# Kernel optimization log

Hardware: AMD Instinct MI355X
Metric: run time of the kernel (lower is better)

The kernel has to match this reference:

```python
import jax, jax.numpy as jnp
import numpy as np

B, T, IN, H, P = 1024, 100, 1, 256, 0.5


def _lstm_scan(xs, h0, c0, Wih, Whh, bih, bhh, mask_h, mask_in=None):
    """Run an LSTMCell over time with variational dropout masks.
    xs: [T, B, D]. mask_h multiplies the recurrent hidden state (as in the
    original: cell(x_t, (h * mask1, c))); mask_in (optional) multiplies input.
    PyTorch LSTMCell gate order: i, f, g, o."""
    b = bih + bhh

    def step(carry, xt):
        h, c = carry
        xin = xt if mask_in is None else xt * mask_in
        g = xin @ Wih.T + (h * mask_h) @ Whh.T + b  # [B, 4H]
        i, f, gg, o = jnp.split(g, 4, axis=-1)
        c = jax.nn.sigmoid(f) * c + jax.nn.sigmoid(i) * jnp.tanh(gg)
        h = jax.nn.sigmoid(o) * jnp.tanh(c)
        return (h, c), h

    _, hs = jax.lax.scan(step, (h0, c0), xs)
    return hs  # [T, B, H]


def setup_inputs() -> dict:
    key = jax.random.key(0)
    ks = jax.random.split(key, 24)
    s = 1.0 / np.sqrt(H)

    def u(k, shape):
        return jax.random.uniform(k, shape, jnp.float32, -s, s)

    inp = {"x0": jax.random.normal(ks[0], (B, T, IN), jnp.float32)}
    names = ["1f", "1b", "2f", "2b"]
    in_sizes = [2 * IN, 2 * IN, 2 * H, 2 * H]
    i = 1
    for n, d in zip(names, in_sizes):
        inp[f"Wih{n}"] = u(ks[i], (4 * H, d)); i += 1
        inp[f"Whh{n}"] = u(ks[i], (4 * H, H)); i += 1
        inp[f"bih{n}"] = u(ks[i], (4 * H,)); i += 1
        inp[f"bhh{n}"] = u(ks[i], (4 * H,)); i += 1
    inp["Wout"] = u(ks[17], (IN, 2 * H))
    inp["bout"] = u(ks[18], (IN,))
    # Variational dropout masks (Bernoulli(1 - dropout_prob)), per set_dropout(batch)
    def bern(k, shape):
        return (jax.random.uniform(k, shape) > P).astype(jnp.float32)
    inp["mask1"] = bern(ks[19], (B, H))
    inp["mask2"] = bern(ks[20], (B, 2 * H))
    inp["mask3"] = bern(ks[21], (B, H))
    inp["mask4"] = bern(ks[22], (B, 1, 2 * H))
    return inp


def reference(x0,
              Wih1f, Whh1f, bih1f, bhh1f,
              Wih1b, Whh1b, bih1b, bhh1b,
              Wih2f, Whh2f, bih2f, bhh2f,
              Wih2b, Whh2b, bih2b, bhh2b,
              Wout, bout, mask1, mask2, mask3, mask4):
    batch = x0.shape[0]
    m = x0.mean(axis=1, keepdims=True)                       # [B, 1, IN]
    x = jnp.concatenate([x0 - m, jnp.broadcast_to(m, x0.shape)], axis=2)  # [B, T, 2*IN]
    xs = jnp.swapaxes(x, 0, 1)                               # [T, B, 2*IN]

    h0 = jnp.zeros((batch, H), x0.dtype)
    c0 = jnp.zeros((batch, H), x0.dtype)

    # Layer 1, forward and backward in time (backward outputs NOT re-flipped,
    # faithful to the original which stacks them in reversed-visit order).
    hf = _lstm_scan(xs, h0, c0, Wih1f, Whh1f, bih1f, bhh1f, mask1)
    hb = _lstm_scan(xs[::-1], h0, c0, Wih1b, Whh1b, bih1b, bhh1b, mask1)
    p1 = jnp.concatenate([hf, hb], axis=-1)                  # [T, B, 2H]

    # Layer 2 with input mask2 and recurrent mask3
    h2f = _lstm_scan(p1, h0, c0, Wih2f, Whh2f, bih2f, bhh2f, mask3, mask_in=mask2)
    h2b = _lstm_scan(p1[::-1], h0, c0, Wih2b, Whh2b, bih2b, bhh2b, mask3, mask_in=mask2)
    p2 = jnp.concatenate([h2f, h2b], axis=-1)                # [T, B, 2H]

    pa = jnp.swapaxes(p2, 0, 1)                              # [B, T, 2H]
    pred = (pa * mask4) @ Wout.T + bout                      # [B, T, IN]
    return pred + m
```

## Files before the change

### kernel.cpp

```cpp
#include <hip/hip_runtime.h>
#include <cstdint>
#include <cstddef>

#define B_  1024
#define T_  100
#define H_  256

typedef _Float16 f16x8 __attribute__((ext_vector_type(8)));
typedef float    f32x16 __attribute__((ext_vector_type(16)));

__device__ __forceinline__ float sigm(float x){ return 1.0f/(1.0f + __expf(-x)); }
__device__ __forceinline__ float tanh_(float x){ return 1.0f - 2.0f/(1.0f + __expf(2.0f*x)); }

#define W_WHH1F 0
#define W_WHH1B 262144
#define W_WIH2F 524288
#define W_WIH2B 1048576
#define W_WHH2F 1572864
#define W_WHH2B 1835008
#define W_TOTAL 2097152

__device__ __forceinline__ void gemm_chunk(
    f32x16 acc[4],
    const _Float16* __restrict__ Asrc, int a_stride,
    const _Float16* __restrict__ Wsrc, int w_stride,
    _Float16* Alds,
    int b0, int j0, int lane, int rw, int cw)
{
  const int t = threadIdx.x;
  #pragma unroll
  for (int i = 0; i < 8; i++){
    int u   = t + 256*i;
    int row = u >> 5;
    int c8  = u & 31;
    uint4 v = *(const uint4*)(Asrc + (size_t)(b0 + row)*a_stride + c8*8);
    *(uint4*)(Alds + row*264 + c8*8) = v;
  }
  __syncthreads();
  const _Float16* arow = Alds + (rw*32 + (lane & 31))*264 + (lane >> 5)*8;
  const int nbase = j0 + cw*32 + (lane & 31);
  const int kq    = (lane >> 5)*8;
  #pragma unroll
  for (int kk = 0; kk < 16; kk++){
    f16x8 a = *(const f16x8*)(arow + kk*16);
    #pragma unroll
    for (int g = 0; g < 4; g++){
      const _Float16* wp = Wsrc + (size_t)(g*256 + nbase)*w_stride + kk*16 + kq;
      f16x8 bw = *(const f16x8*)wp;
      acc[g] = __builtin_amdgcn_mfma_f32_32x32x16_f16(a, bw, acc[g], 0, 0, 0);
    }
  }
  __syncthreads();
}

__global__ void conv_weights(const float* __restrict__ Whh1f, const float* __restrict__ Whh1b,
                             const float* __restrict__ Wih2f, const float* __restrict__ Wih2b,
                             const float* __restrict__ Whh2f, const float* __restrict__ Whh2b,
                             _Float16* __restrict__ dst)
{
  int idx = blockIdx.x*256 + threadIdx.x;
  if      (idx < W_WHH1B) dst[idx] = (_Float16)Whh1f[idx];
  else if (idx < W_WIH2F) dst[idx] = (_Float16)Whh1b[idx - W_WHH1B];
  else if (idx < W_WIH2B) dst[idx] = (_Float16)Wih2f[idx - W_WIH2F];
  else if (idx < W_WHH2F) dst[idx] = (_Float16)Wih2b[idx - W_WIH2B];
  else if (idx < W_WHH2B) dst[idx] = (_Float16)Whh2f[idx - W_WHH2F];
  else if (idx < W_TOTAL) dst[idx] = (_Float16)Whh2b[idx - W_WHH2B];
}

__global__ __launch_bounds__(256, 2)
void l1_step(const _Float16* __restrict__ wpool,
             const float* __restrict__ Wih_f,
             const float* __restrict__ Wih_b,
             const float* __restrict__ bih_f,
             const float* __restrict__ bhh_f,
             const float* __restrict__ bih_b,
             const float* __restrict__ bhh_b,
             const float* __restrict__ x0,
             const float* __restrict__ mvec,
             const float* __restrict__ mask1,
             const float* __restrict__ mask2,
             const _Float16* __restrict__ hm_in,
             _Float16* __restrict__ hm_out,
             float* __restrict__ cbuf,
             _Float16* __restrict__ p1m,
             int s)
{
  __shared__ __align__(16) _Float16 Alds[64*264];
  const int dir = blockIdx.z;
  const int b0  = blockIdx.x*64, j0 = blockIdx.y*64;
  const int lane = threadIdx.x & 63;
  const int w = threadIdx.x >> 6, rw = w >> 1, cw = w & 1;

  f32x16 acc[4];
  #pragma unroll
  for (int g = 0; g < 4; g++)
    #pragma unroll
    for (int e = 0; e < 16; e++) acc[g][e] = 0.0f;

  const _Float16* Whh = wpool + (dir ? W_WHH1B : W_WHH1F);
  gemm_chunk(acc, hm_in + (size_t)dir*B_*H_, H_, Whh, H_, Alds, b0, j0, lane, rw, cw);

  const int tin = dir ? (T_-1-s) : s;
  const float* Wih = dir ? Wih_b : Wih_f;
  const float* bih = dir ? bih_b : bih_f;
  const float* bhh = dir ? bhh_b : bhh_f;
  const int jj = j0 + cw*32 + (lane & 31);

  float wi0[4], wi1[4], bs[4];
  #pragma unroll
  for (int g = 0; g < 4; g++){
    int n = g*256 + jj;
    wi0[g] = Wih[n*2 + 0];
    wi1[g] = Wih[n*2 + 1];
    bs[g]  = bih[n] + bhh[n];
  }
  float* cp = cbuf + (size_t)dir*B_*H_;
  _Float16* hmo = hm_out + (size_t)dir*B_*H_;

  #pragma unroll
  for (int r = 0; r < 16; r++){
    int row = (r & 3) + 8*(r >> 2) + 4*(lane >> 5);
    int b   = b0 + rw*32 + row;
    float mv = mvec[b];
    float xd = x0[b*T_ + tin] - mv;
    float gi = acc[0][r] + xd*wi0[0] + mv*wi1[0] + bs[0];
    float gf = acc[1][r] + xd*wi0[1] + mv*wi1[1] + bs[1];
    float gg = acc[2][r] + xd*wi0[2] + mv*wi1[2] + bs[2];
    float go = acc[3][r] + xd*wi0[3] + mv*wi1[3] + bs[3];
    float ii = sigm(gi), ff = sigm(gf), g2 = tanh_(gg), oo = sigm(go);
    size_t cidx = (size_t)b*H_ + jj;
    float cn = ff*cp[cidx] + ii*g2;
    cp[cidx] = cn;
    float h = oo*tanh_(cn);
    hmo[cidx] = (_Float16)(h * mask1[cidx]);
    p1m[((size_t)s*B_ + b)*512 + dir*256 + jj] =
        (_Float16)(h * mask2[(size_t)b*512 + dir*256 + jj]);
  }
}

__global__ __launch_bounds__(256, 2)
void l2_step(const _Float16* __restrict__ wpool,
             const float* __restrict__ bih_f,
             const float* __restrict__ bhh_f,
             const float* __restrict__ bih_b,
             const float* __restrict__ bhh_b,
             const _Float16* __restrict__ p1m,
             const float* __restrict__ mask3,
             const float* __restrict__ mask4,
             const float* __restrict__ Wout,
             const _Float16* __restrict__ hm_in,
             _Float16* __restrict__ hm_out,
             float* __restrict__ cbuf,
             float* __restrict__ pred,
             int s)
{
  __shared__ __align__(16) _Float16 Alds[64*264];
  const int dir = blockIdx.z;
  const int b0  = blockIdx.x*64, j0 = blockIdx.y*64;
  const int lane = threadIdx.x & 63;
  const int w = threadIdx.x >> 6, rw = w >> 1, cw = w & 1;

  f32x16 acc[4];
  #pragma unroll
  for (int g = 0; g < 4; g++)
    #pragma unroll
    for (int e = 0; e < 16; e++) acc[g][e] = 0.0f;

  const int tin = dir ? (T_-1-s) : s;
  const _Float16* Wih = wpool + (dir ? W_WIH2B : W_WIH2F);
  const _Float16* Whh = wpool + (dir ? W_WHH2B : W_WHH2F);
  const _Float16* Ain = p1m + (size_t)tin*B_*512;

  gemm_chunk(acc, Ain,       512, Wih,       512, Alds, b0, j0, lane, rw, cw);
  gemm_chunk(acc, Ain + 256, 512, Wih + 256, 512, Alds, b0, j0, lane, rw, cw);
  gemm_chunk(acc, hm_in + (size_t)dir*B_*H_, H_, Whh, H_, Alds, b0, j0, lane, rw, cw);

  const float* bih = dir ? bih_b : bih_f;
  const float* bhh = dir ? bhh_b : bhh_f;
  const int jj = j0 + cw*32 + (lane & 31);
  float bs[4];
  #pragma unroll
  for (int g = 0; g < 4; g++)
    bs[g] = bih[g*256 + jj] + bhh[g*256 + jj];
  float wo = Wout[dir*256 + jj];
  float* cp = cbuf + (size_t)dir*B_*H_;
  _Float16* hmo = hm_out + (size_t)dir*B_*H_;

  #pragma unroll
  for (int r = 0; r < 16; r++){
    int row = (r & 3) + 8*(r >> 2) + 4*(lane >> 5);
    int b   = b0 + rw*32 + row;
    float gi = acc[0][r] + bs[0];
    float gf = acc[1][r] + bs[1];
    float gg = acc[2][r] + bs[2];
    float go = acc[3][r] + bs[3];
    float ii = sigm(gi), ff = sigm(gf), g2 = tanh_(gg), oo = sigm(go);
    size_t cidx = (size_t)b*H_ + jj;
    float cn = ff*cp[cidx] + ii*g2;
    cp[cidx] = cn;
    float h = oo*tanh_(cn);
    hmo[cidx] = (_Float16)(h * mask3[cidx]);
    float contrib = h * mask4[(size_t)b*512 + dir*256 + jj] * wo;
    contrib += __shfl_xor(contrib, 16);
    contrib += __shfl_xor(contrib, 8);
    contrib += __shfl_xor(contrib, 4);
    contrib += __shfl_xor(contrib, 2);
    contrib += __shfl_xor(contrib, 1);
    if ((lane & 31) == 0) atomicAdd(&pred[(size_t)b*T_ + s], contrib);
  }
}

__global__ void prep_kernel(const float* __restrict__ x0,
                            float* __restrict__ mvec)
{
  int b = blockIdx.x*blockDim.x + threadIdx.x;
  if (b < B_){
    float ssum = 0.0f;
    for (int t = 0; t < T_; t++) ssum += x0[b*T_ + t];
    mvec[b] = ssum * (1.0f / T_);
  }
}

__global__ void final_kernel(const float* __restrict__ pred,
                             const float* __restrict__ mvec,
                             const float* __restrict__ bout,
                             float* __restrict__ out)
{
  int idx = blockIdx.x*256 + threadIdx.x;
  if (idx < B_*T_){
    int b = idx / T_;
    out[idx] = pred[idx] + bout[0] + mvec[b];
  }
}

extern "C" void kernel_launch(void* const* d_in, const int* in_sizes, int n_in,
                              void* d_out, int out_size, void* d_ws, size_t ws_size,
                              hipStream_t stream)
{
  (void)in_sizes; (void)n_in; (void)out_size; (void)ws_size;
  const float* x0    = (const float*)d_in[0];
  const float* Wih1f = (const float*)d_in[1];
  const float* Whh1f = (const float*)d_in[2];
  const float* bih1f = (const float*)d_in[3];
  const float* bhh1f = (const float*)d_in[4];
  const float* Wih1b = (const float*)d_in[5];
  const float* Whh1b = (const float*)d_in[6];
  const float* bih1b = (const float*)d_in[7];
  const float* bhh1b = (const float*)d_in[8];
  const float* Wih2f = (const float*)d_in[9];
  const float* Whh2f = (const float*)d_in[10];
  const float* bih2f = (const float*)d_in[11];
  const float* bhh2f = (const float*)d_in[12];
  const float* Wih2b = (const float*)d_in[13];
  const float* Whh2b = (const float*)d_in[14];
  const float* bih2b = (const float*)d_in[15];
  const float* bhh2b = (const float*)d_in[16];
  const float* Wout  = (const float*)d_in[17];
  const float* bout  = (const float*)d_in[18];
  const float* mask1 = (const float*)d_in[19];
  const float* mask2 = (const float*)d_in[20];
  const float* mask3 = (const float*)d_in[21];
  const float* mask4 = (const float*)d_in[22];
  float* out = (float*)d_out;

  char* ws = (char*)d_ws;
  size_t off = 0;
  _Float16* wpool = (_Float16*)(ws + off); off += (size_t)W_TOTAL*2;
  _Float16* p1m  = (_Float16*)(ws + off); off += (size_t)T_*B_*512*2;
  float* pred = (float*)(ws + off); off += (size_t)B_*T_*4;
  float* mvec = (float*)(ws + off); off += (size_t)B_*4;
  float* cbuf = (float*)(ws + off); off += (size_t)2*2*B_*H_*4;
  _Float16* hm = (_Float16*)(ws + off); off += (size_t)2*2*2*B_*H_*2;

  hipMemsetAsync(pred, 0, (size_t)B_*T_*4, stream);
  hipMemsetAsync(cbuf, 0, (size_t)2*2*B_*H_*4 + (size_t)2*2*2*B_*H_*2, stream);

  conv_weights<<<dim3(W_TOTAL/256), dim3(256), 0, stream>>>(
      Whh1f, Whh1b, Wih2f, Wih2b, Whh2f, Whh2b, wpool);
  prep_kernel<<<dim3(4), dim3(256), 0, stream>>>(x0, mvec);

  dim3 grid(16, 4, 2), blk(256);
  float* cL1 = cbuf;
  float* cL2 = cbuf + (size_t)2*B_*H_;
  _Float16* hmL1 = hm;
  _Float16* hmL2 = hm + (size_t)2*2*B_*H_;
  const size_t pp = (size_t)2*B_*H_;

  for (int s = 0; s < T_; s++){
    l1_step<<<grid, blk, 0, stream>>>(wpool, Wih1f, Wih1b,
        bih1f, bhh1f, bih1b, bhh1b, x0, mvec, mask1, mask2,
        hmL1 + (size_t)(s & 1)*pp, hmL1 + (size_t)((s + 1) & 1)*pp, cL1, p1m, s);
  }
  for (int s = 0; s < T_; s++){
    l2_step<<<grid, blk, 0, stream>>>(wpool,
        bih2f, bhh2f, bih2b, bhh2b, p1m, mask3, mask4, Wout,
        hmL2 + (size_t)(s & 1)*pp, hmL2 + (size_t)((s + 1) & 1)*pp, cL2, pred, s);
  }
  final_kernel<<<dim3((B_*T_ + 255)/256), dim3(256), 0, stream>>>(pred, mvec, bout, out);
}
```

Before: 5.193 ms.

## Replace per-timestep kernel launches with a persistent kernel using group barriers

The 200 per-step launches for the two LSTM layers are replaced by a single persistent kernel of 256 blocks of 128 threads. Each block owns a 32-row batch tile and a 64-column hidden tile. Blocks sharing a batch tile and direction synchronise each step through atomic counters in global memory, so launch overhead and device-wide step boundaries go away. A global barrier separates layer 1 from layer 2. The smaller tiles halve per-block reuse of the weights, and correctness depends on all 256 blocks being co-resident.

```diff
diff --git a/kernel.cpp b/kernel.cpp
--- a/kernel.cpp
+++ b/kernel.cpp
@@ -19,39 +19,6 @@
 #define W_WHH2F 1572864
 #define W_WHH2B 1835008
 #define W_TOTAL 2097152
-
-__device__ __forceinline__ void gemm_chunk(
-    f32x16 acc[4],
-    const _Float16* __restrict__ Asrc, int a_stride,
-    const _Float16* __restrict__ Wsrc, int w_stride,
-    _Float16* Alds,
-    int b0, int j0, int lane, int rw, int cw)
-{
-  const int t = threadIdx.x;
-  #pragma unroll
-  for (int i = 0; i < 8; i++){
-    int u   = t + 256*i;
-    int row = u >> 5;
-    int c8  = u & 31;
-    uint4 v = *(const uint4*)(Asrc + (size_t)(b0 + row)*a_stride + c8*8);
-    *(uint4*)(Alds + row*264 + c8*8) = v;
-  }
-  __syncthreads();
-  const _Float16* arow = Alds + (rw*32 + (lane & 31))*264 + (lane >> 5)*8;
-  const int nbase = j0 + cw*32 + (lane & 31);
-  const int kq    = (lane >> 5)*8;
-  #pragma unroll
-  for (int kk = 0; kk < 16; kk++){
-    f16x8 a = *(const f16x8*)(arow + kk*16);
-    #pragma unroll
-    for (int g = 0; g < 4; g++){
-      const _Float16* wp = Wsrc + (size_t)(g*256 + nbase)*w_stride + kk*16 + kq;
-      f16x8 bw = *(const f16x8*)wp;
-      acc[g] = __builtin_amdgcn_mfma_f32_32x32x16_f16(a, bw, acc[g], 0, 0, 0);
-    }
-  }
-  __syncthreads();
-}
 
 __global__ void conv_weights(const float* __restrict__ Whh1f, const float* __restrict__ Whh1b,
                              const float* __restrict__ Wih2f, const float* __restrict__ Wih2b,
@@ -67,152 +34,7 @@
   else if (idx < W_TOTAL) dst[idx] = (_Float16)Whh2b[idx - W_WHH2B];
 }
 
-__global__ __launch_bounds__(256, 2)
-void l1_step(const _Float16* __restrict__ wpool,
-             const float* __restrict__ Wih_f,
-             const float* __restrict__ Wih_b,
-             const float* __restrict__ bih_f,
-             const float* __restrict__ bhh_f,
-             const float* __restrict__ bih_b,
-             const float* __restrict__ bhh_b,
-             const float* __restrict__ x0,
-             const float* __restrict__ mvec,
-             const float* __restrict__ mask1,
-             const float* __restrict__ mask2,
-             const _Float16* __restrict__ hm_in,
-             _Float16* __restrict__ hm_out,
-             float* __restrict__ cbuf,
-             _Float16* __restrict__ p1m,
-             int s)
-{
-  __shared__ __align__(16) _Float16 Alds[64*264];
-  const int dir = blockIdx.z;
-  const int b0  = blockIdx.x*64, j0 = blockIdx.y*64;
-  const int lane = threadIdx.x & 63;
-  const int w = threadIdx.x >> 6, rw = w >> 1, cw = w & 1;
-
-  f32x16 acc[4];
-  #pragma unroll
-  for (int g = 0; g < 4; g++)
-    #pragma unroll
-    for (int e = 0; e < 16; e++) acc[g][e] = 0.0f;
-
-  const _Float16* Whh = wpool + (dir ? W_WHH1B : W_WHH1F);
-  gemm_chunk(acc, hm_in + (size_t)dir*B_*H_, H_, Whh, H_, Alds, b0, j0, lane, rw, cw);
-
-  const int tin = dir ? (T_-1-s) : s;
-  const float* Wih = dir ? Wih_b : Wih_f;
-  const float* bih = dir ? bih_b : bih_f;
-  const float* bhh = dir ? bhh_b : bhh_f;
-  const int jj = j0 + cw*32 + (lane & 31);
-
-  float wi0[4], wi1[4], bs[4];
-  #pragma unroll
-  for (int g = 0; g < 4; g++){
-    int n = g*256 + jj;
-    wi0[g] = Wih[n*2 + 0];
-    wi1[g] = Wih[n*2 + 1];
-    bs[g]  = bih[n] + bhh[n];
-  }
-  float* cp = cbuf + (size_t)dir*B_*H_;
-  _Float16* hmo = hm_out + (size_t)dir*B_*H_;
-
-  #pragma unroll
-  for (int r = 0; r < 16; r++){
-    int row = (r & 3) + 8*(r >> 2) + 4*(lane >> 5);
-    int b   = b0 + rw*32 + row;
-    float mv = mvec[b];
-    float xd = x0[b*T_ + tin] - mv;
-    float gi = acc[0][r] + xd*wi0[0] + mv*wi1[0] + bs[0];
-    float gf = acc[1][r] + xd*wi0[1] + mv*wi1[1] + bs[1];
-    float gg = acc[2][r] + xd*wi0[2] + mv*wi1[2] + bs[2];
-    float go = acc[3][r] + xd*wi0[3] + mv*wi1[3] + bs[3];
-    float ii = sigm(gi), ff = sigm(gf), g2 = tanh_(gg), oo = sigm(go);
-    size_t cidx = (size_t)b*H_ + jj;
-    float cn = ff*cp[cidx] + ii*g2;
-    cp[cidx] = cn;
-    float h = oo*tanh_(cn);
-    hmo[cidx] = (_Float16)(h * mask1[cidx]);
-    p1m[((size_t)s*B_ + b)*512 + dir*256 + jj] =
-        (_Float16)(h * mask2[(size_t)b*512 + dir*256 + jj]);
-  }
-}
-
-__global__ __launch_bounds__(256, 2)
-void l2_step(const _Float16* __restrict__ wpool,
-             const float* __restrict__ bih_f,
-             const float* __restrict__ bhh_f,
-             const float* __restrict__ bih_b,
-             const float* __restrict__ bhh_b,
-             const _Float16* __restrict__ p1m,
-             const float* __restrict__ mask3,
-             const float* __restrict__ mask4,
-             const float* __restrict__ Wout,
-             const _Float16* __restrict__ hm_in,
-             _Float16* __restrict__ hm_out,
-             float* __restrict__ cbuf,
-             float* __restrict__ pred,
-             int s)
-{
-  __shared__ __align__(16) _Float16 Alds[64*264];
-  const int dir = blockIdx.z;
-  const int b0  = blockIdx.x*64, j0 = blockIdx.y*64;
-  const int lane = threadIdx.x & 63;
-  const int w = threadIdx.x >> 6, rw = w >> 1, cw = w & 1;
-
-  f32x16 acc[4];
-  #pragma unroll
-  for (int g = 0; g < 4; g++)
-    #pragma unroll
-    for (int e = 0; e < 16; e++) acc[g][e] = 0.0f;
-
-  const int tin = dir ? (T_-1-s) : s;
-  const _Float16* Wih = wpool + (dir ? W_WIH2B : W_WIH2F);
-  const _Float16* Whh = wpool + (dir ? W_WHH2B : W_WHH2F);
-  const _Float16* Ain = p1m + (size_t)tin*B_*512;
-
-  gemm_chunk(acc, Ain,       512, Wih,       512, Alds, b0, j0, lane, rw, cw);
-  gemm_chunk(acc, Ain + 256, 512, Wih + 256, 512, Alds, b0, j0, lane, rw, cw);
-  gemm_chunk(acc, hm_in + (size_t)dir*B_*H_, H_, Whh, H_, Alds, b0, j0, lane, rw, cw);
-
-  const float* bih = dir ? bih_b : bih_f;
-  const float* bhh = dir ? bhh_b : bhh_f;
-  const int jj = j0 + cw*32 + (lane & 31);
-  float bs[4];
-  #pragma unroll
-  for (int g = 0; g < 4; g++)
-    bs[g] = bih[g*256 + jj] + bhh[g*256 + jj];
-  float wo = Wout[dir*256 + jj];
-  float* cp = cbuf + (size_t)dir*B_*H_;
-  _Float16* hmo = hm_out + (size_t)dir*B_*H_;
-
-  #pragma unroll
-  for (int r = 0; r < 16; r++){
-    int row = (r & 3) + 8*(r >> 2) + 4*(lane >> 5);
-    int b   = b0 + rw*32 + row;
-    float gi = acc[0][r] + bs[0];
-    float gf = acc[1][r] + bs[1];
-    float gg = acc[2][r] + bs[2];
-    float go = acc[3][r] + bs[3];
-    float ii = sigm(gi), ff = sigm(gf), g2 = tanh_(gg), oo = sigm(go);
-    size_t cidx = (size_t)b*H_ + jj;
-    float cn = ff*cp[cidx] + ii*g2;
-    cp[cidx] = cn;
-    float h = oo*tanh_(cn);
-    hmo[cidx] = (_Float16)(h * mask3[cidx]);
-    float contrib = h * mask4[(size_t)b*512 + dir*256 + jj] * wo;
-    contrib += __shfl_xor(contrib, 16);
-    contrib += __shfl_xor(contrib, 8);
-    contrib += __shfl_xor(contrib, 4);
-    contrib += __shfl_xor(contrib, 2);
-    contrib += __shfl_xor(contrib, 1);
-    if ((lane & 31) == 0) atomicAdd(&pred[(size_t)b*T_ + s], contrib);
-  }
-}
-
-__global__ void prep_kernel(const float* __restrict__ x0,
-                            float* __restrict__ mvec)
-{
+__global__ void prep_kernel(const float* __restrict__ x0, float* __restrict__ mvec){
   int b = blockIdx.x*blockDim.x + threadIdx.x;
   if (b < B_){
     float ssum = 0.0f;
@@ -221,15 +43,187 @@
   }
 }
 
-__global__ void final_kernel(const float* __restrict__ pred,
-                             const float* __restrict__ mvec,
-                             const float* __restrict__ bout,
-                             float* __restrict__ out)
-{
+__global__ void final_kernel(const float* __restrict__ pred, const float* __restrict__ mvec,
+                             const float* __restrict__ bout, float* __restrict__ out){
   int idx = blockIdx.x*256 + threadIdx.x;
   if (idx < B_*T_){
     int b = idx / T_;
     out[idx] = pred[idx] + bout[0] + mvec[b];
+  }
+}
+
+struct PP {
+  const float *x0, *Wih1f, *Wih1b, *b1f_ih, *b1f_hh, *b1b_ih, *b1b_hh;
+  const float *b2f_ih, *b2f_hh, *b2b_ih, *b2b_hh;
+  const float *Wout, *mask1, *mask2, *mask3, *mask4;
+  const _Float16 *wpool;
+  _Float16 *p1m, *hm1, *hm2;
+  float *cbuf1, *cbuf2, *pred, *mvec;
+  unsigned *ctr1, *ctr2, *ctrF;
+};
+
+__device__ __forceinline__ void bar_wait(unsigned* c, unsigned target){
+  __syncthreads();
+  if (threadIdx.x == 0){
+    __threadfence();
+    __hip_atomic_fetch_add(c, 1u, __ATOMIC_RELEASE, __HIP_MEMORY_SCOPE_AGENT);
+    while (__hip_atomic_load(c, __ATOMIC_ACQUIRE, __HIP_MEMORY_SCOPE_AGENT) < target)
+      __builtin_amdgcn_s_sleep(8);
+  }
+  __syncthreads();
+  __threadfence();
+}
+
+__device__ __forceinline__ void gemm32(
+    f32x16 acc[4],
+    const _Float16* __restrict__ Asrc, int a_stride,
+    const _Float16* __restrict__ Wsrc, int w_stride,
+    _Float16* Alds,
+    int b0, int j0, int cw, int ln31, int lhi)
+{
+  const int t = threadIdx.x;
+  #pragma unroll
+  for (int i = 0; i < 8; i++){
+    int u   = t + 128*i;
+    int row = u >> 5;
+    int c8  = u & 31;
+    uint4 v = *(const uint4*)(Asrc + (size_t)(b0 + row)*a_stride + c8*8);
+    *(uint4*)(Alds + row*264 + c8*8) = v;
+  }
+  __syncthreads();
+  const _Float16* arow = Alds + ln31*264 + lhi*8;
+  const int nbase = j0 + cw*32 + ln31;
+  const int kq    = lhi*8;
+  #pragma unroll
+  for (int kk = 0; kk < 16; kk++){
+    f16x8 a = *(const f16x8*)(arow + kk*16);
+    #pragma unroll
+    for (int g = 0; g < 4; g++){
+      const _Float16* wp = Wsrc + (size_t)(g*256 + nbase)*w_stride + kk*16 + kq;
+      f16x8 bw = *(const f16x8*)wp;
+      acc[g] = __builtin_amdgcn_mfma_f32_32x32x16_f16(a, bw, acc[g], 0, 0, 0);
+    }
+  }
+  __syncthreads();
+}
+
+__global__ __launch_bounds__(128) void lstm_persist(PP p){
+  __shared__ __align__(16) _Float16 Alds[32*264];
+  const int btile = blockIdx.x;
+  const int j0    = blockIdx.y*64;
+  const int dir   = blockIdx.z;
+  const int b0    = btile*32;
+  const int grp   = dir*32 + btile;
+  const int lane  = threadIdx.x & 63;
+  const int cw    = threadIdx.x >> 6;
+  const int ln31  = lane & 31, lhi = lane >> 5;
+  const int jj    = j0 + cw*32 + ln31;
+
+  {
+    const _Float16* Whh = p.wpool + (dir ? W_WHH1B : W_WHH1F);
+    const float* Wih = dir ? p.Wih1b : p.Wih1f;
+    const float* bih = dir ? p.b1b_ih : p.b1f_ih;
+    const float* bhh = dir ? p.b1b_hh : p.b1f_hh;
+    float wi0[4], wi1[4], bs[4];
+    #pragma unroll
+    for (int g = 0; g < 4; g++){
+      int n = g*256 + jj;
+      wi0[g] = Wih[n*2 + 0];
+      wi1[g] = Wih[n*2 + 1];
+      bs[g]  = bih[n] + bhh[n];
+    }
+    float* cp = p.cbuf1 + (size_t)dir*B_*H_;
+
+    for (int s = 0; s < T_; s++){
+      const _Float16* hmcur = p.hm1 + (size_t)((s & 1)*2 + dir)*B_*H_;
+      _Float16* hmnxt = p.hm1 + (size_t)(((s+1) & 1)*2 + dir)*B_*H_;
+      const int tin = dir ? (T_-1-s) : s;
+
+      f32x16 acc[4];
+      #pragma unroll
+      for (int g = 0; g < 4; g++)
+        #pragma unroll
+        for (int e = 0; e < 16; e++) acc[g][e] = 0.0f;
+
+      gemm32(acc, hmcur, H_, Whh, H_, Alds, b0, j0, cw, ln31, lhi);
+
+      #pragma unroll
+      for (int r = 0; r < 16; r++){
+        int row = (r & 3) + 8*(r >> 2) + 4*lhi;
+        int b   = b0 + row;
+        float mv = p.mvec[b];
+        float xd = p.x0[b*T_ + tin] - mv;
+        float gi = acc[0][r] + xd*wi0[0] + mv*wi1[0] + bs[0];
+        float gf = acc[1][r] + xd*wi0[1] + mv*wi1[1] + bs[1];
+        float gg = acc[2][r] + xd*wi0[2] + mv*wi1[2] + bs[2];
+        float go = acc[3][r] + xd*wi0[3] + mv*wi1[3] + bs[3];
+        float ii = sigm(gi), ff = sigm(gf), g2 = tanh_(gg), oo = sigm(go);
+        size_t ci = (size_t)b*H_ + jj;
+        float cn = ff*cp[ci] + ii*g2;
+        cp[ci] = cn;
+        float h = oo*tanh_(cn);
+        hmnxt[ci] = (_Float16)(h * p.mask1[ci]);
+        p.p1m[((size_t)s*B_ + b)*512 + dir*256 + jj] =
+            (_Float16)(h * p.mask2[(size_t)b*512 + dir*256 + jj]);
+      }
+      if (s < T_-1) bar_wait(&p.ctr1[grp*16], (unsigned)(s+1)*4);
+    }
+  }
+
+  bar_wait(p.ctrF, 256u);
+
+  {
+    const _Float16* Wih = p.wpool + (dir ? W_WIH2B : W_WIH2F);
+    const _Float16* Whh = p.wpool + (dir ? W_WHH2B : W_WHH2F);
+    const float* bih = dir ? p.b2b_ih : p.b2f_ih;
+    const float* bhh = dir ? p.b2b_hh : p.b2f_hh;
+    float bs[4];
+    #pragma unroll
+    for (int g = 0; g < 4; g++)
+      bs[g] = bih[g*256 + jj] + bhh[g*256 + jj];
+    float wo = p.Wout[dir*256 + jj];
+    float* cp = p.cbuf2 + (size_t)dir*B_*H_;
+
+    for (int s = 0; s < T_; s++){
+      const int tin = dir ? (T_-1-s) : s;
+      const _Float16* Ain = p.p1m + (size_t)tin*B_*512;
+      const _Float16* hmcur = p.hm2 + (size_t)((s & 1)*2 + dir)*B_*H_;
+      _Float16* hmnxt = p.hm2 + (size_t)(((s+1) & 1)*2 + dir)*B_*H_;
+
+      f32x16 acc[4];
+      #pragma unroll
+      for (int g = 0; g < 4; g++)
+        #pragma unroll
+        for (int e = 0; e < 16; e++) acc[g][e] = 0.0f;
+
+      gemm32(acc, Ain,       512, Wih,       512, Alds, b0, j0, cw, ln31, lhi);
+      gemm32(acc, Ain + 256, 512, Wih + 256, 512, Alds, b0, j0, cw, ln31, lhi);
+      gemm32(acc, hmcur,     H_,  Whh,       H_,  Alds, b0, j0, cw, ln31, lhi);
+
+      #pragma unroll
+      for (int r = 0; r < 16; r++){
+        int row = (r & 3) + 8*(r >> 2) + 4*lhi;
+        int b   = b0 + row;
+        float gi = acc[0][r] + bs[0];
+        float gf = acc[1][r] + bs[1];
+        float gg = acc[2][r] + bs[2];
+        float go = acc[3][r] + bs[3];
+        float ii = sigm(gi), ff = sigm(gf), g2 = tanh_(gg), oo = sigm(go);
+        size_t ci = (size_t)b*H_ + jj;
+        float cn = ff*cp[ci] + ii*g2;
+        cp[ci] = cn;
+        float h = oo*tanh_(cn);
+        hmnxt[ci] = (_Float16)(h * p.mask3[ci]);
+        float contrib = h * p.mask4[(size_t)b*512 + dir*256 + jj] * wo;
+        contrib += __shfl_xor(contrib, 16);
+        contrib += __shfl_xor(contrib, 8);
+        contrib += __shfl_xor(contrib, 4);
+        contrib += __shfl_xor(contrib, 2);
+        contrib += __shfl_xor(contrib, 1);
+        if (ln31 == 0) atomicAdd(&p.pred[(size_t)b*T_ + s], contrib);
+      }
+      if (s < T_-1) bar_wait(&p.ctr2[grp*16], (unsigned)(s+1)*4);
+    }
   }
 }
 
@@ -266,35 +260,35 @@
   char* ws = (char*)d_ws;
   size_t off = 0;
   _Float16* wpool = (_Float16*)(ws + off); off += (size_t)W_TOTAL*2;
-  _Float16* p1m  = (_Float16*)(ws + off); off += (size_t)T_*B_*512*2;
-  float* pred = (float*)(ws + off); off += (size_t)B_*T_*4;
-  float* mvec = (float*)(ws + off); off += (size_t)B_*4;
-  float* cbuf = (float*)(ws + off); off += (size_t)2*2*B_*H_*4;
-  _Float16* hm = (_Float16*)(ws + off); off += (size_t)2*2*2*B_*H_*2;
-
-  hipMemsetAsync(pred, 0, (size_t)B_*T_*4, stream);
-  hipMemsetAsync(cbuf, 0, (size_t)2*2*B_*H_*4 + (size_t)2*2*2*B_*H_*2, stream);
-
+  _Float16* p1m   = (_Float16*)(ws + off); off += (size_t)T_*B_*512*2;
+  char* zbase = ws + off;
+  float* pred  = (float*)(ws + off); off += (size_t)B_*T_*4;
+  float* mvec  = (float*)(ws + off); off += (size_t)B_*4;
+  float* cbuf1 = (float*)(ws + off); off += (size_t)2*B_*H_*4;
+  float* cbuf2 = (float*)(ws + off); off += (size_t)2*B_*H_*4;
+  _Float16* hm1 = (_Float16*)(ws + off); off += (size_t)2*2*B_*H_*2;
+  _Float16* hm2 = (_Float16*)(ws + off); off += (size_t)2*2*B_*H_*2;
+  unsigned* ctr1 = (unsigned*)(ws + off); off += 64*16*4;
+  unsigned* ctr2 = (unsigned*)(ws + off); off += 64*16*4;
+  unsigned* ctrF = (unsigned*)(ws + off); off += 64;
+  size_t zbytes = (size_t)((ws + off) - zbase);
+
+  hipMemsetAsync(zbase, 0, zbytes, stream);
   conv_weights<<<dim3(W_TOTAL/256), dim3(256), 0, stream>>>(
       Whh1f, Whh1b, Wih2f, Wih2b, Whh2f, Whh2b, wpool);
   prep_kernel<<<dim3(4), dim3(256), 0, stream>>>(x0, mvec);
 
-  dim3 grid(16, 4, 2), blk(256);
-  float* cL1 = cbuf;
-  float* cL2 = cbuf + (size_t)2*B_*H_;
-  _Float16* hmL1 = hm;
-  _Float16* hmL2 = hm + (size_t)2*2*B_*H_;
-  const size_t pp = (size_t)2*B_*H_;
-
-  for (int s = 0; s < T_; s++){
-    l1_step<<<grid, blk, 0, stream>>>(wpool, Wih1f, Wih1b,
-        bih1f, bhh1f, bih1b, bhh1b, x0, mvec, mask1, mask2,
-        hmL1 + (size_t)(s & 1)*pp, hmL1 + (size_t)((s + 1) & 1)*pp, cL1, p1m, s);
-  }
-  for (int s = 0; s < T_; s++){
-    l2_step<<<grid, blk, 0, stream>>>(wpool,
-        bih2f, bhh2f, bih2b, bhh2b, p1m, mask3, mask4, Wout,
-        hmL2 + (size_t)(s & 1)*pp, hmL2 + (size_t)((s + 1) & 1)*pp, cL2, pred, s);
-  }
+  PP prm;
+  prm.x0 = x0; prm.Wih1f = Wih1f; prm.Wih1b = Wih1b;
+  prm.b1f_ih = bih1f; prm.b1f_hh = bhh1f; prm.b1b_ih = bih1b; prm.b1b_hh = bhh1b;
+  prm.b2f_ih = bih2f; prm.b2f_hh = bhh2f; prm.b2b_ih = bih2b; prm.b2b_hh = bhh2b;
+  prm.Wout = Wout; prm.mask1 = mask1; prm.mask2 = mask2; prm.mask3 = mask3; prm.mask4 = mask4;
+  prm.wpool = wpool;
+  prm.p1m = p1m; prm.hm1 = hm1; prm.hm2 = hm2;
+  prm.cbuf1 = cbuf1; prm.cbuf2 = cbuf2; prm.pred = pred; prm.mvec = mvec;
+  prm.ctr1 = ctr1; prm.ctr2 = ctr2; prm.ctrF = ctrF;
+
+  lstm_persist<<<dim3(32, 4, 2), dim3(128), 0, stream>>>(prm);
+
   final_kernel<<<dim3((B_*T_ + 255)/256), dim3(256), 0, stream>>>(pred, mvec, bout, out);
 }
```

After: 10.40 ms. 2x slower.
